# Kernel tuning notes

Measured on AMD Instinct MI355X. Metric: run time of the kernel, lower is better.

The kernel has to match this reference:

```python
import jax, jax.numpy as jnp
import numpy as np

W_BIT, OUT_F, IN_F, K = 4, 4096, 4096, 16
B, S = 4, 2048


def setup_inputs() -> dict:
    key = jax.random.key(0)
    k1, k2, k3, k4 = jax.random.split(key, 4)
    x = jax.random.normal(k1, (B, S, IN_F), dtype=jnp.float16)
    # bit-packed signs: 8 signs per byte, stored as int32 in [0, 256)
    qweight = jax.random.randint(k2, (W_BIT, OUT_F * IN_F // 8), 0, 256, dtype=jnp.int32)
    u = jax.random.normal(k3, (W_BIT, OUT_F, K), dtype=jnp.float16) * jnp.float16(0.1)
    vt = jax.random.normal(k4, (W_BIT, K, IN_F), dtype=jnp.float16) * jnp.float16(0.1)
    return {"x": x, "qweight": qweight, "u": u, "vt": vt}


def _unpack_sign(qweight, out_f, in_f, dtype):
    # [w_bit, N/8] packed bytes -> [w_bit, out_f, in_f] signs in {-1, +1}
    bits = (qweight[:, :, None] >> jnp.arange(8, dtype=qweight.dtype)) & 1
    sign = (2 * bits - 1).reshape(qweight.shape[0], out_f, in_f)
    return sign.astype(dtype)


def reference(x, qweight, u, vt):
    w_bit, out_f, _ = u.shape
    in_f = vt.shape[2]
    sign = _unpack_sign(qweight, out_f, in_f, u.dtype)          # [w_bit, out, in]
    lowrank = jnp.einsum('bok,bki->boi', u, vt)                  # per-bit u @ vt
    w = jnp.sum(sign * lowrank, axis=0)                          # [out, in]
    return x @ w.T                                               # [B, S, out]
```

## Files before the change

kernel.cpp:

```cpp
#include <hip/hip_runtime.h>
#include <stdint.h>


#define W_BITS 4
#define OUT_F  4096
#define IN_F   4096
#define K_RANK 16
#define M_TOT  8192
#define QW_PER_BIT (OUT_F * IN_F / 8)

typedef __attribute__((ext_vector_type(8))) short bf16x8;
typedef __attribute__((ext_vector_type(4))) float f32x4;

__device__ __forceinline__ unsigned short f2bf(float f) {
  union { float f; unsigned int u; } c; c.f = f;
  unsigned int r = c.u + 0x7fffu + ((c.u >> 16) & 1u);
  return (unsigned short)(r >> 16);
}

__global__ __launch_bounds__(256) void convert_x(
    const float* __restrict__ X, unsigned short* __restrict__ Xb, int n8)
{
  const int stride = gridDim.x * blockDim.x;
  for (int i = blockIdx.x * blockDim.x + threadIdx.x; i < n8; i += stride) {
    const f32x4 a = *reinterpret_cast<const f32x4*>(X + (size_t)i * 8);
    const f32x4 b = *reinterpret_cast<const f32x4*>(X + (size_t)i * 8 + 4);
    unsigned short o8[8] = {f2bf(a[0]), f2bf(a[1]), f2bf(a[2]), f2bf(a[3]),
                            f2bf(b[0]), f2bf(b[1]), f2bf(b[2]), f2bf(b[3])};
    *reinterpret_cast<uint4*>(Xb + (size_t)i * 8) = *reinterpret_cast<const uint4*>(o8);
  }
}

#define TO 4

__global__ __launch_bounds__(256) void build_w(
    const int*   __restrict__ qw,
    const float* __restrict__ u,
    const float* __restrict__ vt,
    unsigned short* __restrict__ w)
{
  const int tid = blockIdx.x * 256 + threadIdx.x;
  const int ig  = tid & 511;
  const int i0  = ig << 3;
  const int ob  = (tid >> 9) << 2;

  float acc[TO][8];
  #pragma unroll
  for (int t = 0; t < TO; ++t)
    #pragma unroll
    for (int ii = 0; ii < 8; ++ii) acc[t][ii] = 0.0f;

  #pragma unroll
  for (int bit = 0; bit < W_BITS; ++bit) {
    float lr[TO][8];
    #pragma unroll
    for (int t = 0; t < TO; ++t)
      #pragma unroll
      for (int ii = 0; ii < 8; ++ii) lr[t][ii] = 0.0f;

    const float* vbase = vt + (size_t)(bit * K_RANK) * IN_F + i0;
    const float* ubase = u + (size_t)(bit * OUT_F + ob) * K_RANK;

    #pragma unroll
    for (int k = 0; k < K_RANK; ++k) {
      const f32x4 v0 = *reinterpret_cast<const f32x4*>(vbase + (size_t)k * IN_F);
      const f32x4 v1 = *reinterpret_cast<const f32x4*>(vbase + (size_t)k * IN_F + 4);
      float vf[8] = {v0[0], v0[1], v0[2], v0[3], v1[0], v1[1], v1[2], v1[3]};
      #pragma unroll
      for (int t = 0; t < TO; ++t) {
        const float uk = ubase[t * K_RANK + k];
        #pragma unroll
        for (int ii = 0; ii < 8; ++ii) lr[t][ii] += uk * vf[ii];
      }
    }

    #pragma unroll
    for (int t = 0; t < TO; ++t) {
      const int q = qw[(size_t)bit * QW_PER_BIT + (size_t)(ob + t) * (IN_F / 8) + ig];
      #pragma unroll
      for (int ii = 0; ii < 8; ++ii)
        acc[t][ii] += ((q >> ii) & 1) ? lr[t][ii] : -lr[t][ii];
    }
  }

  #pragma unroll
  for (int t = 0; t < TO; ++t) {
    unsigned short o8[8];
    #pragma unroll
    for (int ii = 0; ii < 8; ++ii) o8[ii] = f2bf(acc[t][ii]);
    *reinterpret_cast<uint4*>(w + (size_t)(ob + t) * IN_F + i0) =
        *reinterpret_cast<const uint4*>(o8);
  }
}

__device__ __forceinline__ void gll16(unsigned short* lds, const unsigned short* g) {
  __builtin_amdgcn_global_load_lds(
      (const __attribute__((address_space(1))) unsigned int*)g,
      (__attribute__((address_space(3))) unsigned int*)lds,
      16, 0, 0);
}

__global__ __launch_bounds__(512, 2) void gemm_256(
    const unsigned short* __restrict__ X,
    const unsigned short* __restrict__ W,
    float* __restrict__ out)
{
  __shared__ __align__(16) unsigned short Al[2][256][64];
  __shared__ __align__(16) unsigned short Bl[2][256][64];

  const int bid = blockIdx.x;
  const int swz = (bid & 7) * 64 + (bid >> 3);
  const int bm = swz >> 4;
  const int bn = swz & 15;

  const int tid  = threadIdx.x;
  const int lane = tid & 63;
  const int wid  = tid >> 6;
  const int wm   = wid >> 2;
  const int wn   = wid & 3;

  const int sr = tid >> 3;
  const int sc = (((tid & 7) ^ (sr & 7)) << 3);

  const unsigned short* Abase = X + (size_t)(bm * 256 + sr) * IN_F + sc;
  const unsigned short* Bbase = W + (size_t)(bn * 256 + sr) * IN_F + sc;
  unsigned short* Alt = &Al[0][0][0] + tid * 8;
  unsigned short* Blt = &Bl[0][0][0] + tid * 8;

  const int fr  = lane & 15;
  const int sw0 = (((lane >> 4) ^ (fr & 7)) << 3);
  const int aRow = (wm * 16 + fr) * 64;
  const int bRow = (wn * 16 + fr) * 64;
  const unsigned short* Ar = &Al[0][0][0];
  const unsigned short* Br = &Bl[0][0][0];

  f32x4 acc[8][4];
  #pragma unroll
  for (int f = 0; f < 8; ++f)
    #pragma unroll
    for (int g = 0; g < 4; ++g)
      acc[f][g] = (f32x4){0.f, 0.f, 0.f, 0.f};

#define STAGE(buf, h, tn_) do {                                                        \
    const unsigned short* gs_ = ((h) < 2 ? Abase : Bbase)                              \
        + (size_t)(((h) & 1) * 128) * IN_F + (size_t)(tn_) * 64;                       \
    unsigned short* ld_ = ((h) < 2 ? Alt : Blt) + (buf) * 16384 + ((h) & 1) * 8192;    \
    gll16(ld_, gs_);                                                                   \
    gll16(ld_ + 4096, gs_ + (size_t)64 * IN_F);                                        \
  } while (0)

#define WAITBAR() do {                                                                 \
    asm volatile("s_waitcnt vmcnt(6)" ::: "memory");                                   \
    __builtin_amdgcn_s_barrier();                                                      \
    __builtin_amdgcn_sched_barrier(0);                                                 \
  } while (0)

#define LGKMW(n_) do {                                                                 \
    asm volatile("s_waitcnt lgkmcnt(" #n_ ")" ::: "memory");                           \
    __builtin_amdgcn_sched_barrier(0);                                                 \
  } while (0)

#define SB() __builtin_amdgcn_sched_barrier(0)

#define RD_A(base_, mh_, f_, ks_)                                                      \
    aF[f_][ks_] = *reinterpret_cast<const bf16x8*>(                                    \
        Ar + (base_) + ((mh_) * 4 + (f_)) * 2048 + aRow + (((ks_) * 32) ^ sw0))

#define RD_B(dst_, base_, nh_, g_, ks_)                                                \
    dst_[g_][ks_] = *reinterpret_cast<const bf16x8*>(                                  \
        Br + (base_) + ((nh_) * 2 + (g_)) * 4096 + bRow + (((ks_) * 32) ^ sw0))

#define MF(mh_, nh_, f_, g_, ks_, bsrc_)                                               \
    acc[(mh_) * 4 + (f_)][(nh_) * 2 + (g_)] = __builtin_amdgcn_mfma_f32_16x16x32_bf16( \
        aF[f_][ks_], bsrc_[g_][ks_], acc[(mh_) * 4 + (f_)][(nh_) * 2 + (g_)], 0, 0, 0)

#define MF4(mh_, nh_, f_, bsrc_) do {                                                  \
    MF(mh_, nh_, f_, 0, 0, bsrc_); MF(mh_, nh_, f_, 0, 1, bsrc_);                      \
    MF(mh_, nh_, f_, 1, 0, bsrc_); MF(mh_, nh_, f_, 1, 1, bsrc_); } while (0)

#define KTILE(P_, Q_, CC_, OO_, tn1_, tn2_) do {                                       \
    const int cb_ = (CC_) * 16384, ob_ = (OO_) * 16384;                                \
              \
    STAGE(OO_, 1, tn1_);                                                               \
    WAITBAR();                                                                         \
    LGKMW(0);                                                                          \
    __builtin_amdgcn_s_setprio(1);                                                     \
    MF4(0, 0, 0, P_); MF4(0, 0, 1, P_); MF4(0, 0, 2, P_); MF4(0, 0, 3, P_);            \
    __builtin_amdgcn_s_setprio(0);                                                     \
    SB();                                                                              \
    RD_B(Q_, cb_, 1, 0, 0); RD_B(Q_, cb_, 1, 0, 1);                                    \
    RD_B(Q_, cb_, 1, 1, 0); RD_B(Q_, cb_, 1, 1, 1);                                    \
             \
    STAGE(OO_, 3, tn1_);                                                               \
    WAITBAR();                                                                         \
    LGKMW(0);                                                                          \
    __builtin_amdgcn_s_setprio(1);                                                     \
    MF4(0, 1, 0, Q_); MF4(0, 1, 1, Q_); MF4(0, 1, 2, Q_); MF4(0, 1, 3, Q_);            \
    __builtin_amdgcn_s_setprio(0);                                                     \
    SB();                                                                              \
    RD_A(cb_, 1, 0, 0); RD_A(cb_, 1, 0, 1); RD_A(cb_, 1, 1, 0); RD_A(cb_, 1, 1, 1);    \
    RD_A(cb_, 1, 2, 0); RD_A(cb_, 1, 2, 1); RD_A(cb_, 1, 3, 0); RD_A(cb_, 1, 3, 1);    \
             \
    STAGE(CC_, 2, tn2_);                                                               \
    WAITBAR();                                                                         \
    LGKMW(0);                                                                          \
    __builtin_amdgcn_s_setprio(1);                                                     \
    MF4(1, 1, 0, Q_); MF4(1, 1, 1, Q_); MF4(1, 1, 2, Q_); MF4(1, 1, 3, Q_);            \
    __builtin_amdgcn_s_setprio(0);                                                     \
    SB();                                                                              \
    RD_B(Q_, ob_, 0, 0, 0); RD_B(Q_, ob_, 0, 0, 1);                                    \
    RD_B(Q_, ob_, 0, 1, 0); RD_B(Q_, ob_, 0, 1, 1);                                    \
            \
    STAGE(CC_, 0, tn2_);                                                               \
    WAITBAR();                                                                         \
    LGKMW(0);                                                                          \
    __builtin_amdgcn_s_setprio(1);                                                     \
    MF4(1, 0, 0, P_); MF4(1, 0, 1, P_); MF4(1, 0, 2, P_); MF4(1, 0, 3, P_);            \
    __builtin_amdgcn_s_setprio(0);                                                     \
    SB();                                                                              \
    RD_A(ob_, 0, 0, 0); RD_A(ob_, 0, 0, 1); RD_A(ob_, 0, 1, 0); RD_A(ob_, 0, 1, 1);    \
    RD_A(ob_, 0, 2, 0); RD_A(ob_, 0, 2, 1); RD_A(ob_, 0, 3, 0); RD_A(ob_, 0, 3, 1);    \
  } while (0)

  STAGE(0, 2, 0);
  STAGE(0, 0, 0);
  STAGE(0, 1, 0);
  STAGE(0, 3, 0);
  STAGE(1, 2, 1);
  STAGE(1, 0, 1);
  asm volatile("s_waitcnt vmcnt(8)" ::: "memory");
  __builtin_amdgcn_s_barrier();
  __builtin_amdgcn_sched_barrier(0);

  bf16x8 aF[4][2], bF0[2][2], bF1[2][2];
  RD_A(0, 0, 0, 0); RD_A(0, 0, 0, 1); RD_A(0, 0, 1, 0); RD_A(0, 0, 1, 1);
  RD_A(0, 0, 2, 0); RD_A(0, 0, 2, 1); RD_A(0, 0, 3, 0); RD_A(0, 0, 3, 1);
  RD_B(bF0, 0, 0, 0, 0); RD_B(bF0, 0, 0, 0, 1);
  RD_B(bF0, 0, 0, 1, 0); RD_B(bF0, 0, 0, 1, 1);

  #pragma unroll 1
  for (int Th = 0; Th < 32; ++Th) {
    const int T0 = 2 * Th;
    const int tA1 = (T0 + 1 < 64) ? T0 + 1 : 63;
    const int tA2 = (T0 + 2 < 64) ? T0 + 2 : 63;
    const int tB1 = (T0 + 2 < 64) ? T0 + 2 : 63;
    const int tB2 = (T0 + 3 < 64) ? T0 + 3 : 63;
    KTILE(bF0, bF1, 0, 1, tA1, tA2);
    KTILE(bF1, bF0, 1, 0, tB1, tB2);
  }

  asm volatile("s_waitcnt vmcnt(0) lgkmcnt(0)" ::: "memory");

  const int rsub = (lane >> 4) << 2;
  #pragma unroll
  for (int f = 0; f < 8; ++f) {
    const int row = bm * 256 + (f * 2 + wm) * 16 + rsub;
    #pragma unroll
    for (int g = 0; g < 4; ++g) {
      const int col = bn * 256 + (g * 4 + wn) * 16 + (lane & 15);
      float* op = out + (size_t)row * OUT_F + col;
      #pragma unroll
      for (int j = 0; j < 4; ++j) op[(size_t)j * OUT_F] = acc[f][g][j];
    }
  }
#undef STAGE
#undef WAITBAR
#undef LGKMW
#undef SB
#undef RD_A
#undef RD_B
#undef MF
#undef MF4
#undef KTILE
}

#define BM 128
#define BN 128
#define BK 32

__device__ __forceinline__ uint4 cvt8(f32x4 a, f32x4 b) {
  unsigned short o8[8] = {f2bf(a[0]), f2bf(a[1]), f2bf(a[2]), f2bf(a[3]),
                          f2bf(b[0]), f2bf(b[1]), f2bf(b[2]), f2bf(b[3])};
  return *reinterpret_cast<const uint4*>(o8);
}

__global__ __launch_bounds__(256) void gemm_f32stage(
    const float* __restrict__ X,
    const unsigned short* __restrict__ W,
    float* __restrict__ out)
{
  __shared__ __align__(16) unsigned short As[BM * BK];
  __shared__ __align__(16) unsigned short Bs[BN * BK];

  const int nbn = OUT_F / BN;
  const int cpx = (M_TOT / BM) * nbn / 8;
  const int bid = blockIdx.x;
  const int swz = (bid & 7) * cpx + (bid >> 3);
  const int bm = swz / nbn;
  const int bn = swz % nbn;

  const int tid  = threadIdx.x;
  const int lane = tid & 63;
  const int wid  = tid >> 6;
  const int wm   = wid >> 1;
  const int wn   = wid & 1;
  const int srow = tid >> 2;
  const int scol = (tid & 3) << 3;

  const float*          Ag = X + (size_t)(bm * BM + srow) * IN_F + scol;
  const unsigned short* Bg = W + (size_t)(bn * BN + srow) * IN_F + scol;

  const int fr = lane & 15;
  const int fk = (lane >> 4) << 3;

  f32x4 acc[4][4];
  #pragma unroll
  for (int m = 0; m < 4; ++m)
    #pragma unroll
    for (int n = 0; n < 4; ++n)
      acc[m][n] = (f32x4){0.f, 0.f, 0.f, 0.f};

  for (int k0 = 0; k0 < IN_F; k0 += BK) {
    const f32x4 a0a = *reinterpret_cast<const f32x4*>(Ag + k0);
    const f32x4 a0b = *reinterpret_cast<const f32x4*>(Ag + k0 + 4);
    const f32x4 a1a = *reinterpret_cast<const f32x4*>(Ag + (size_t)64 * IN_F + k0);
    const f32x4 a1b = *reinterpret_cast<const f32x4*>(Ag + (size_t)64 * IN_F + k0 + 4);
    const uint4 b0  = *reinterpret_cast<const uint4*>(Bg + k0);
    const uint4 b1  = *reinterpret_cast<const uint4*>(Bg + (size_t)64 * IN_F + k0);

    __syncthreads();
    *reinterpret_cast<uint4*>(As + tid * 8)        = cvt8(a0a, a0b);
    *reinterpret_cast<uint4*>(As + 2048 + tid * 8) = cvt8(a1a, a1b);
    *reinterpret_cast<uint4*>(Bs + tid * 8)        = b0;
    *reinterpret_cast<uint4*>(Bs + 2048 + tid * 8) = b1;
    __syncthreads();

    bf16x8 af[4], bfv[4];
    #pragma unroll
    for (int m = 0; m < 4; ++m)
      af[m] = *reinterpret_cast<const bf16x8*>(&As[(wm * 64 + m * 16 + fr) * BK + fk]);
    #pragma unroll
    for (int n = 0; n < 4; ++n)
      bfv[n] = *reinterpret_cast<const bf16x8*>(&Bs[(wn * 64 + n * 16 + fr) * BK + fk]);

    #pragma unroll
    for (int m = 0; m < 4; ++m)
      #pragma unroll
      for (int n = 0; n < 4; ++n)
        acc[m][n] = __builtin_amdgcn_mfma_f32_16x16x32_bf16(af[m], bfv[n], acc[m][n], 0, 0, 0);
  }

  const int rsub = (lane >> 4) << 2;
  #pragma unroll
  for (int m = 0; m < 4; ++m) {
    #pragma unroll
    for (int n = 0; n < 4; ++n) {
      const int col = bn * BN + wn * 64 + n * 16 + (lane & 15);
      #pragma unroll
      for (int j = 0; j < 4; ++j) {
        const int row = bm * BM + wm * 64 + m * 16 + rsub + j;
        out[(size_t)row * OUT_F + col] = acc[m][n][j];
      }
    }
  }
}

extern "C" void kernel_launch(void* const* d_in, const int* in_sizes, int n_in,
                              void* d_out, int out_size, void* d_ws, size_t ws_size,
                              hipStream_t stream) {
  (void)in_sizes; (void)n_in; (void)out_size;

  const float* x  = (const float*)d_in[0];
  const int*   qw = (const int*)d_in[1];
  const float* u  = (const float*)d_in[2];
  const float* vt = (const float*)d_in[3];
  float* out = (float*)d_out;

  unsigned short* w = (unsigned short*)d_ws;
  const size_t W_BYTES  = (size_t)OUT_F * IN_F * 2;
  const size_t XB_BYTES = (size_t)M_TOT * IN_F * 2;

  build_w<<<dim3(2048), dim3(256), 0, stream>>>(qw, u, vt, w);

  if (ws_size >= W_BYTES + XB_BYTES) {
    unsigned short* xb = w + (size_t)OUT_F * IN_F;
    convert_x<<<dim3(2048), dim3(256), 0, stream>>>(x, xb, M_TOT * IN_F / 8);
    gemm_256<<<dim3(512), dim3(512), 0, stream>>>(xb, w, out);
  } else {
    gemm_f32stage<<<dim3(2048), dim3(256), 0, stream>>>(x, w, out);
  }
}
```

Baseline: 366.9 us.

## Restructure GEMM k-loop pipeline with in-tile LDS reads and double barriers

Reworks the main bf16 MFMA GEMM loop schedule. Each k-tile now reads its own A/B fragments from LDS at the start instead of prefetching the next tile's fragments across the tile boundary. The global-to-LDS stage order is rearranged, with a single vmcnt wait per tile instead of one per quarter. Barriers are added after each MFMA group. The aim is to cut vmcnt stalls and give the global loads more time in flight, at the cost of more barriers and less overlap of LDS reads with MFMAs.

```diff
diff --git a/kernel.cpp b/kernel.cpp
--- a/kernel.cpp
+++ b/kernel.cpp
@@ -149,19 +149,19 @@
     gll16(ld_ + 4096, gs_ + (size_t)64 * IN_F);                                        \
   } while (0)
 
-#define WAITBAR() do {                                                                 \
-    asm volatile("s_waitcnt vmcnt(6)" ::: "memory");                                   \
+#define LGKMW0() do {                                                                  \
+    asm volatile("s_waitcnt lgkmcnt(0)" ::: "memory");                                 \
+    __builtin_amdgcn_sched_barrier(0);                                                 \
+  } while (0)
+
+#define SB() __builtin_amdgcn_sched_barrier(0)
+
+#define BAR() do {                                                                     \
+    __builtin_amdgcn_sched_barrier(0);                                                 \
     __builtin_amdgcn_s_barrier();                                                      \
     __builtin_amdgcn_sched_barrier(0);                                                 \
   } while (0)
 
-#define LGKMW(n_) do {                                                                 \
-    asm volatile("s_waitcnt lgkmcnt(" #n_ ")" ::: "memory");                           \
-    __builtin_amdgcn_sched_barrier(0);                                                 \
-  } while (0)
-
-#define SB() __builtin_amdgcn_sched_barrier(0)
-
 #define RD_A(base_, mh_, f_, ks_)                                                      \
     aF[f_][ks_] = *reinterpret_cast<const bf16x8*>(                                    \
         Ar + (base_) + ((mh_) * 4 + (f_)) * 2048 + aRow + (((ks_) * 32) ^ sw0))
@@ -178,75 +178,76 @@
     MF(mh_, nh_, f_, 0, 0, bsrc_); MF(mh_, nh_, f_, 0, 1, bsrc_);                      \
     MF(mh_, nh_, f_, 1, 0, bsrc_); MF(mh_, nh_, f_, 1, 1, bsrc_); } while (0)
 
-#define KTILE(P_, Q_, CC_, OO_, tn1_, tn2_) do {                                       \
-    const int cb_ = (CC_) * 16384, ob_ = (OO_) * 16384;                                \
-              \
-    STAGE(OO_, 1, tn1_);                                                               \
-    WAITBAR();                                                                         \
-    LGKMW(0);                                                                          \
+#define KTILE(CC_, OO_, tn1_, tn2_) do {                                               \
+    const int cb_ = (CC_) * 16384;                                                     \
+             \
+    RD_A(cb_, 0, 0, 0); RD_A(cb_, 0, 0, 1); RD_A(cb_, 0, 1, 0); RD_A(cb_, 0, 1, 1);    \
+    RD_A(cb_, 0, 2, 0); RD_A(cb_, 0, 2, 1); RD_A(cb_, 0, 3, 0); RD_A(cb_, 0, 3, 1);    \
+    RD_B(bF0, cb_, 0, 0, 0); RD_B(bF0, cb_, 0, 0, 1);                                  \
+    RD_B(bF0, cb_, 0, 1, 0); RD_B(bF0, cb_, 0, 1, 1);                                  \
+    SB();                                                                              \
+    STAGE(OO_, 2, tn1_);                                                               \
+    BAR();                                                                             \
+    LGKMW0();                                                                          \
     __builtin_amdgcn_s_setprio(1);                                                     \
-    MF4(0, 0, 0, P_); MF4(0, 0, 1, P_); MF4(0, 0, 2, P_); MF4(0, 0, 3, P_);            \
+    MF4(0, 0, 0, bF0); MF4(0, 0, 1, bF0); MF4(0, 0, 2, bF0); MF4(0, 0, 3, bF0);        \
     __builtin_amdgcn_s_setprio(0);                                                     \
+    BAR();                                                                             \
+                        \
+    RD_B(bF1, cb_, 1, 0, 0); RD_B(bF1, cb_, 1, 0, 1);                                  \
+    RD_B(bF1, cb_, 1, 1, 0); RD_B(bF1, cb_, 1, 1, 1);                                  \
     SB();                                                                              \
-    RD_B(Q_, cb_, 1, 0, 0); RD_B(Q_, cb_, 1, 0, 1);                                    \
-    RD_B(Q_, cb_, 1, 1, 0); RD_B(Q_, cb_, 1, 1, 1);                                    \
-             \
-    STAGE(OO_, 3, tn1_);                                                               \
-    WAITBAR();                                                                         \
-    LGKMW(0);                                                                          \
+    STAGE(CC_, 0, tn2_);                                                               \
+    BAR();                                                                             \
+    LGKMW0();                                                                          \
     __builtin_amdgcn_s_setprio(1);                                                     \
-    MF4(0, 1, 0, Q_); MF4(0, 1, 1, Q_); MF4(0, 1, 2, Q_); MF4(0, 1, 3, Q_);            \
+    MF4(0, 1, 0, bF1); MF4(0, 1, 1, bF1); MF4(0, 1, 2, bF1); MF4(0, 1, 3, bF1);        \
     __builtin_amdgcn_s_setprio(0);                                                     \
-    SB();                                                                              \
+    BAR();                                                                             \
+                         \
     RD_A(cb_, 1, 0, 0); RD_A(cb_, 1, 0, 1); RD_A(cb_, 1, 1, 0); RD_A(cb_, 1, 1, 1);    \
     RD_A(cb_, 1, 2, 0); RD_A(cb_, 1, 2, 1); RD_A(cb_, 1, 3, 0); RD_A(cb_, 1, 3, 1);    \
-             \
-    STAGE(CC_, 2, tn2_);                                                               \
-    WAITBAR();                                                                         \
-    LGKMW(0);                                                                          \
+    SB();                                                                              \
+    STAGE(CC_, 3, tn2_);                                                               \
+    BAR();                                                                             \
+    LGKMW0();                                                                          \
     __builtin_amdgcn_s_setprio(1);                                                     \
-    MF4(1, 1, 0, Q_); MF4(1, 1, 1, Q_); MF4(1, 1, 2, Q_); MF4(1, 1, 3, Q_);            \
+    MF4(1, 1, 0, bF1); MF4(1, 1, 1, bF1); MF4(1, 1, 2, bF1); MF4(1, 1, 3, bF1);        \
     __builtin_amdgcn_s_setprio(0);                                                     \
-    SB();                                                                              \
-    RD_B(Q_, ob_, 0, 0, 0); RD_B(Q_, ob_, 0, 0, 1);                                    \
-    RD_B(Q_, ob_, 0, 1, 0); RD_B(Q_, ob_, 0, 1, 1);                                    \
-            \
-    STAGE(CC_, 0, tn2_);                                                               \
-    WAITBAR();                                                                         \
-    LGKMW(0);                                                                          \
+    BAR();                                                                             \
+                           \
+    STAGE(CC_, 1, tn2_);                                                               \
+    asm volatile("s_waitcnt vmcnt(6)" ::: "memory");                                   \
+    BAR();                                                                             \
+    LGKMW0();                                                                          \
     __builtin_amdgcn_s_setprio(1);                                                     \
-    MF4(1, 0, 0, P_); MF4(1, 0, 1, P_); MF4(1, 0, 2, P_); MF4(1, 0, 3, P_);            \
+    MF4(1, 0, 0, bF0); MF4(1, 0, 1, bF0); MF4(1, 0, 2, bF0); MF4(1, 0, 3, bF0);        \
     __builtin_amdgcn_s_setprio(0);                                                     \
-    SB();                                                                              \
-    RD_A(ob_, 0, 0, 0); RD_A(ob_, 0, 0, 1); RD_A(ob_, 0, 1, 0); RD_A(ob_, 0, 1, 1);    \
-    RD_A(ob_, 0, 2, 0); RD_A(ob_, 0, 2, 1); RD_A(ob_, 0, 3, 0); RD_A(ob_, 0, 3, 1);    \
+    BAR();                                                                             \
   } while (0)
 
+  STAGE(0, 0, 0);
+  STAGE(0, 3, 0);
+  STAGE(0, 1, 0);
   STAGE(0, 2, 0);
-  STAGE(0, 0, 0);
-  STAGE(0, 1, 0);
-  STAGE(0, 3, 0);
-  STAGE(1, 2, 1);
   STAGE(1, 0, 1);
-  asm volatile("s_waitcnt vmcnt(8)" ::: "memory");
+  STAGE(1, 3, 1);
+  STAGE(1, 1, 1);
+  asm volatile("s_waitcnt vmcnt(6)" ::: "memory");
   __builtin_amdgcn_s_barrier();
   __builtin_amdgcn_sched_barrier(0);
 
   bf16x8 aF[4][2], bF0[2][2], bF1[2][2];
-  RD_A(0, 0, 0, 0); RD_A(0, 0, 0, 1); RD_A(0, 0, 1, 0); RD_A(0, 0, 1, 1);
-  RD_A(0, 0, 2, 0); RD_A(0, 0, 2, 1); RD_A(0, 0, 3, 0); RD_A(0, 0, 3, 1);
-  RD_B(bF0, 0, 0, 0, 0); RD_B(bF0, 0, 0, 0, 1);
-  RD_B(bF0, 0, 0, 1, 0); RD_B(bF0, 0, 0, 1, 1);
 
   #pragma unroll 1
   for (int Th = 0; Th < 32; ++Th) {
     const int T0 = 2 * Th;
-    const int tA1 = (T0 + 1 < 64) ? T0 + 1 : 63;
-    const int tA2 = (T0 + 2 < 64) ? T0 + 2 : 63;
-    const int tB1 = (T0 + 2 < 64) ? T0 + 2 : 63;
-    const int tB2 = (T0 + 3 < 64) ? T0 + 3 : 63;
-    KTILE(bF0, bF1, 0, 1, tA1, tA2);
-    KTILE(bF1, bF0, 1, 0, tB1, tB2);
+    const int e_t1 = T0 + 1;
+    const int e_t2 = (T0 + 2 < 64) ? T0 + 2 : 63;
+    const int o_t1 = (T0 + 2 < 64) ? T0 + 2 : 63;
+    const int o_t2 = (T0 + 3 < 64) ? T0 + 3 : 63;
+    KTILE(0, 1, e_t1, e_t2);
+    KTILE(1, 0, o_t1, o_t2);
   }
 
   asm volatile("s_waitcnt vmcnt(0) lgkmcnt(0)" ::: "memory");
@@ -264,9 +265,9 @@
     }
   }
 #undef STAGE
-#undef WAITBAR
-#undef LGKMW
+#undef LGKMW0
 #undef SB
+#undef BAR
 #undef RD_A
 #undef RD_B
 #undef MF
```

Result: faster. 359.6 us (-2.0%).
